# Kernel optimization log

Hardware: AMD Instinct MI355X
Metric: run time of the kernel (lower is better)

Reference implementation:

```python
import jax, jax.numpy as jnp
import numpy as np

B, L, D = 2, 2048, 1024
H = 16
HD = D // H  # 64


def setup_inputs() -> dict:
    key = jax.random.key(0)
    ks = jax.random.split(key, 7)
    s = 0.02
    return {
        "x": jax.random.normal(ks[0], (B, L, D), dtype=jnp.float32),
        "Wq": jax.random.normal(ks[1], (D, D), dtype=jnp.float32) * s,
        "bq": jnp.zeros((D,), dtype=jnp.float32),
        "Wkv": jax.random.normal(ks[2], (D, 2 * D), dtype=jnp.float32) * s,
        "bkv": jnp.zeros((2 * D,), dtype=jnp.float32),
        "Wo": jax.random.normal(ks[3], (D, D), dtype=jnp.float32) * s,
        "bo": jnp.zeros((D,), dtype=jnp.float32),
    }


def reference(x, Wq, bq, Wkv, bkv, Wo, bo):
    # q/kv projections (self-attention: key/value come from x)
    q = x @ Wq + bq                      # [B, L, D]
    kv = x @ Wkv + bkv                   # [B, L, 2D]
    k, v = jnp.split(kv, 2, axis=-1)     # each [B, L, D]
    # split heads: 'b l (h c) -> b h l c' (rope_embed_fraction=0 -> RoPE is identity)
    def heads(t):
        return t.reshape(B, L, H, HD).transpose(0, 2, 1, 3)
    qh, kh, vh = heads(q), heads(k), heads(v)   # [B, H, L, HD]
    scale = 1.0 / jnp.sqrt(jnp.asarray(HD, dtype=x.dtype))
    scores = jnp.einsum('bhqc,bhkc->bhqk', qh, kh) * scale  # [B, H, L, L]
    attn = jax.nn.softmax(scores, axis=-1)
    y = jnp.einsum('bhqk,bhkc->bhqc', attn, vh)             # [B, H, L, HD]
    # merge heads: 'b h l c -> b l (h c)'
    y = y.transpose(0, 2, 1, 3).reshape(B, L, D)
    return (y @ Wo + bo).reshape(x.shape)
```

## Files before the change

kernel.cpp:

```cpp
#include <hip/hip_runtime.h>

#define B_  2
#define L_  2048
#define D_  1024
#define H_  16
#define HD_ 64

typedef __attribute__((ext_vector_type(8))) short bf16x8;
typedef __attribute__((ext_vector_type(4))) float f32x4;
typedef __attribute__((ext_vector_type(16))) float f32x16;

#define MFMA16(a, b, c) __builtin_amdgcn_mfma_f32_16x16x32_bf16(a, b, c, 0, 0, 0)
#define MFMA32(a, b, c) __builtin_amdgcn_mfma_f32_32x32x16_bf16(a, b, c, 0, 0, 0)

__device__ __forceinline__ unsigned short f2bf(float f) {
    union { float f; unsigned u; } v; v.f = f;
    unsigned r = v.u + 0x7FFFu + ((v.u >> 16) & 1u);
    return (unsigned short)(r >> 16);
}

__device__ __forceinline__ unsigned pkbf(float a, float b) {
    union { float f; unsigned u; } x, y; x.f = a; y.f = b;
    return __builtin_amdgcn_perm(y.u, x.u, 0x07060302u);
}

__global__ __launch_bounds__(256) void convert_bf16(
    const float* __restrict__ in, unsigned short* __restrict__ out, int n4)
{
    for (int i = blockIdx.x * blockDim.x + threadIdx.x; i < n4;
         i += gridDim.x * blockDim.x) {
        float4 v = *(const float4*)(in + (size_t)i * 4);
        ushort4 u;
        u.x = f2bf(v.x); u.y = f2bf(v.y); u.z = f2bf(v.z); u.w = f2bf(v.w);
        *(ushort4*)(out + (size_t)i * 4) = u;
    }
}

__global__ __launch_bounds__(256) void prep_w(
    const float* __restrict__ Wq, const float* __restrict__ Wkv,
    const float* __restrict__ Wo,
    unsigned short* __restrict__ Wqt, unsigned short* __restrict__ Wkvt,
    unsigned short* __restrict__ Wot)
{
    __shared__ float t[32][33];
    const int z = blockIdx.z;
    const float* W;  unsigned short* Wt;  int N, nc;
    if (z == 0)      { W = Wq;  Wt = Wqt;  N = 1024; nc = 0; }
    else if (z == 1) { W = Wo;  Wt = Wot;  N = 1024; nc = 0; }
    else             { W = Wkv; Wt = Wkvt; N = 2048; nc = (z - 2) * 1024; }
    const int tx = threadIdx.x & 31, ty = threadIdx.x >> 5;
    const int n0 = nc + blockIdx.x * 32, k0 = blockIdx.y * 32;
    #pragma unroll
    for (int r = 0; r < 4; ++r)
        t[ty + r * 8][tx] = W[(size_t)(k0 + ty + r * 8) * N + n0 + tx];
    __syncthreads();
    #pragma unroll
    for (int r = 0; r < 4; ++r)
        Wt[(size_t)(n0 + ty + r * 8) * 1024 + k0 + tx] = f2bf(t[tx][ty + r * 8]);
}

__global__ __launch_bounds__(512, 1) void gemm_qkv8(
    const unsigned short* __restrict__ A,
    const unsigned short* __restrict__ Bt,
    const float* __restrict__ bq, const float* __restrict__ bkv,
    unsigned short* __restrict__ Qb, unsigned short* __restrict__ Kb,
    unsigned short* __restrict__ Vtg, float qscl)
{
    const int KDIM = 1024, NT = 16;
    __shared__ __align__(16) unsigned short lds[65536];

    const int tid = threadIdx.x;
    const int w = tid >> 6, l = tid & 63, g = l >> 4, ln = l & 15;
    const int wm = (w >> 2) & 1, wn = w & 3;

    const int lin = blockIdx.x;
    const int wg = (lin & 7) * 24 + (lin >> 3);
    const int by = wg / 12, bx = wg % 12;
    const int m0 = by * 256, n0 = bx * 256;

    const int sr8 = w * 8 + (l >> 3);
    const int sc  = (l & 7) ^ ((l >> 3) & 7);
    const unsigned short* Asrc = A  + (size_t)m0 * KDIM + sc * 8;
    const unsigned short* Bsrc = Bt + (size_t)n0 * KDIM + sc * 8;

#define SLOT_A(d, h) (lds + ((d) * 2 + (h)) * 8192)
#define SLOT_B(d, h) (lds + 32768 + ((d) * 2 + (h)) * 8192)

#define STG(slotp, srcp, hh, kt_) do {                                        \
    _Pragma("unroll")                                                         \
    for (int r_ = 0; r_ < 2; ++r_) {                                          \
        const int row_ = (hh) * 128 + r_ * 64 + sr8;                          \
        __builtin_amdgcn_global_load_lds(                                     \
            (const __attribute__((address_space(1))) void*)                   \
                ((srcp) + (size_t)row_ * KDIM + (kt_) * 64),                  \
            (__attribute__((address_space(3))) void*)                         \
                ((slotp) + r_ * 4096 + w * 512 + l * 8),                      \
            16, 0, 0);                                                        \
    }                                                                         \
} while (0)

    f32x4 acc[8][4];
    #pragma unroll
    for (int i = 0; i < 8; ++i)
        #pragma unroll
        for (int j = 0; j < 4; ++j) acc[i][j] = (f32x4){0.f, 0.f, 0.f, 0.f};

    bf16x8 aR[4][2], bB0[2][2], bB1[2][2];

    STG(SLOT_A(0, 0), Asrc, 0, 0);
    STG(SLOT_B(0, 1), Bsrc, 1, 0);
    STG(SLOT_A(0, 1), Asrc, 1, 0);
    STG(SLOT_B(0, 0), Bsrc, 0, 0);
    STG(SLOT_A(1, 0), Asrc, 0, 1);
    STG(SLOT_B(1, 1), Bsrc, 1, 1);

    #pragma unroll 1
    for (int kt = 0; kt < NT; ++kt) {
        const int cur = kt & 1, nxt = cur ^ 1;
        asm volatile("s_waitcnt vmcnt(4)" ::: "memory");
        __builtin_amdgcn_s_barrier();

        #pragma unroll
        for (int mi = 0; mi < 4; ++mi)
            #pragma unroll
            for (int kc = 0; kc < 2; ++kc) {
                const int rho = wm * 64 + mi * 16 + ln, c = kc * 4 + g;
                aR[mi][kc] = *(const bf16x8*)
                    (SLOT_A(cur, 0) + rho * 64 + ((c ^ (rho & 7)) * 8));
            }
        #pragma unroll
        for (int ni = 0; ni < 2; ++ni)
            #pragma unroll
            for (int kc = 0; kc < 2; ++kc) {
                const int rho = wn * 32 + ni * 16 + ln, c = kc * 4 + g;
                bB0[ni][kc] = *(const bf16x8*)
                    (SLOT_B(cur, 0) + rho * 64 + ((c ^ (rho & 7)) * 8));
            }
        if (kt + 1 < NT) STG(SLOT_A(nxt, 1), Asrc, 1, kt + 1);
        __builtin_amdgcn_s_barrier();
        asm volatile("s_waitcnt lgkmcnt(0)" ::: "memory");
        __builtin_amdgcn_s_setprio(1);
        #pragma unroll
        for (int mi = 0; mi < 4; ++mi)
            #pragma unroll
            for (int ni = 0; ni < 2; ++ni) {
                acc[mi][ni] = MFMA16(aR[mi][0], bB0[ni][0], acc[mi][ni]);
                acc[mi][ni] = MFMA16(aR[mi][1], bB0[ni][1], acc[mi][ni]);
            }
        __builtin_amdgcn_s_setprio(0);
        __builtin_amdgcn_s_barrier();

        #pragma unroll
        for (int ni = 0; ni < 2; ++ni)
            #pragma unroll
            for (int kc = 0; kc < 2; ++kc) {
                const int rho = wn * 32 + ni * 16 + ln, c = kc * 4 + g;
                bB1[ni][kc] = *(const bf16x8*)
                    (SLOT_B(cur, 1) + rho * 64 + ((c ^ (rho & 7)) * 8));
            }
        if (kt + 1 < NT) STG(SLOT_B(nxt, 0), Bsrc, 0, kt + 1);
        __builtin_amdgcn_s_barrier();
        asm volatile("s_waitcnt lgkmcnt(0)" ::: "memory");
        __builtin_amdgcn_s_setprio(1);
        #pragma unroll
        for (int mi = 0; mi < 4; ++mi)
            #pragma unroll
            for (int ni = 0; ni < 2; ++ni) {
                acc[mi][2 + ni] = MFMA16(aR[mi][0], bB1[ni][0], acc[mi][2 + ni]);
                acc[mi][2 + ni] = MFMA16(aR[mi][1], bB1[ni][1], acc[mi][2 + ni]);
            }
        __builtin_amdgcn_s_setprio(0);
        __builtin_amdgcn_s_barrier();

        #pragma unroll
        for (int mi = 0; mi < 4; ++mi)
            #pragma unroll
            for (int kc = 0; kc < 2; ++kc) {
                const int rho = wm * 64 + mi * 16 + ln, c = kc * 4 + g;
                aR[mi][kc] = *(const bf16x8*)
                    (SLOT_A(cur, 1) + rho * 64 + ((c ^ (rho & 7)) * 8));
            }
        if (kt + 2 < NT) STG(SLOT_A(cur, 0), Asrc, 0, kt + 2);
        __builtin_amdgcn_s_barrier();
        asm volatile("s_waitcnt lgkmcnt(0)" ::: "memory");
        __builtin_amdgcn_s_setprio(1);
        #pragma unroll
        for (int mi = 0; mi < 4; ++mi)
            #pragma unroll
            for (int ni = 0; ni < 2; ++ni) {
                acc[4 + mi][2 + ni] = MFMA16(aR[mi][0], bB1[ni][0], acc[4 + mi][2 + ni]);
                acc[4 + mi][2 + ni] = MFMA16(aR[mi][1], bB1[ni][1], acc[4 + mi][2 + ni]);
            }
        __builtin_amdgcn_s_setprio(0);
        __builtin_amdgcn_s_barrier();

        if (kt + 2 < NT) STG(SLOT_B(cur, 1), Bsrc, 1, kt + 2);
        __builtin_amdgcn_s_barrier();
        __builtin_amdgcn_s_setprio(1);
        #pragma unroll
        for (int mi = 0; mi < 4; ++mi)
            #pragma unroll
            for (int ni = 0; ni < 2; ++ni) {
                acc[4 + mi][ni] = MFMA16(aR[mi][0], bB0[ni][0], acc[4 + mi][ni]);
                acc[4 + mi][ni] = MFMA16(aR[mi][1], bB0[ni][1], acc[4 + mi][ni]);
            }
        __builtin_amdgcn_s_setprio(0);
        __builtin_amdgcn_s_barrier();
    }
#undef STG
#undef SLOT_A
#undef SLOT_B

    const int region = n0 >> 10;
    if (region == 2) {
        #pragma unroll
        for (int nh = 0; nh < 2; ++nh)
            #pragma unroll
            for (int ni = 0; ni < 2; ++ni) {
                const int d = n0 - 2048 + nh * 128 + wn * 32 + ni * 16 + ln;
                const float bv = bkv[1024 + d];
                #pragma unroll
                for (int mh = 0; mh < 2; ++mh)
                    #pragma unroll
                    for (int mi = 0; mi < 4; ++mi) {
                        const int tok = m0 + mh * 128 + wm * 64 + mi * 16 + g * 4;
                        const int bb = tok >> 11, t4 = tok & 2047;
                        const f32x4 av = acc[mh * 4 + mi][nh * 2 + ni];
                        ushort4 p4;
                        p4.x = f2bf(av[0] + bv); p4.y = f2bf(av[1] + bv);
                        p4.z = f2bf(av[2] + bv); p4.w = f2bf(av[3] + bv);
                        *(ushort4*)(Vtg + ((size_t)bb * 1024 + d) * 2048 + t4) = p4;
                    }
            }
    } else {
        const int isQ = (region == 0);
        const float osc = isQ ? qscl : 1.f;
        #pragma unroll
        for (int nh = 0; nh < 2; ++nh)
            #pragma unroll
            for (int ni = 0; ni < 2; ++ni) {
                const int col = n0 + nh * 128 + wn * 32 + ni * 16 + ln;
                const float bv = isQ ? bq[col] : bkv[col - 1024];
                const int ck = isQ ? col : col - 1024;
                #pragma unroll
                for (int mh = 0; mh < 2; ++mh)
                    #pragma unroll
                    for (int mi = 0; mi < 4; ++mi) {
                        const int row = m0 + mh * 128 + wm * 64 + mi * 16 + g * 4;
                        const f32x4 av = acc[mh * 4 + mi][nh * 2 + ni];
                        #pragma unroll
                        for (int r = 0; r < 4; ++r) {
                            const float vout = (av[r] + bv) * osc;
                            if (isQ)
                                Qb[(size_t)(row + r) * 1024 + ck] = f2bf(vout);
                            else
                                Kb[(size_t)(row + r) * 1024 + ck] = f2bf(vout);
                        }
                    }
            }
    }
}

__global__ __launch_bounds__(256) void gemm_bt(
    const unsigned short* __restrict__ A,
    const unsigned short* __restrict__ Bt,
    const float* __restrict__ bias,
    float* __restrict__ Cout, int M, int N, int K)
{
    __shared__ __align__(16) unsigned short As[128 * 32];
    __shared__ __align__(16) unsigned short Bs[128 * 32];
    const int tid = threadIdx.x;
    const int w = tid >> 6, l = tid & 63, g = l >> 4, ln = l & 15;
    const int wm = w >> 1, wn = w & 1;
    const int m0 = blockIdx.y * 128, n0 = blockIdx.x * 128;

    f32x4 acc[4][4];
    #pragma unroll
    for (int i = 0; i < 4; ++i)
        #pragma unroll
        for (int j = 0; j < 4; ++j) acc[i][j] = (f32x4){0.f, 0.f, 0.f, 0.f};

    const char* Ab = (const char*)A;
    const char* Bb = (const char*)Bt;
    const size_t strideK = (size_t)K * 2;

    for (int k0 = 0; k0 < K; k0 += 32) {
        #pragma unroll
        for (int i = 0; i < 2; ++i) {
            const int b = w * 2048 + i * 1024 + l * 16;
            const int row = b >> 6, cb = b & 63;
            __builtin_amdgcn_global_load_lds(
                (const __attribute__((address_space(1))) void*)
                    (Ab + (size_t)(m0 + row) * strideK + (size_t)k0 * 2 + cb),
                (__attribute__((address_space(3))) void*)
                    ((char*)As + w * 2048 + i * 1024),
                16, 0, 0);
            __builtin_amdgcn_global_load_lds(
                (const __attribute__((address_space(1))) void*)
                    (Bb + (size_t)(n0 + row) * strideK + (size_t)k0 * 2 + cb),
                (__attribute__((address_space(3))) void*)
                    ((char*)Bs + w * 2048 + i * 1024),
                16, 0, 0);
        }
        __syncthreads();
        bf16x8 af[4], bfr[4];
        #pragma unroll
        for (int m = 0; m < 4; ++m)
            af[m] = *(const bf16x8*)(As + (wm * 64 + m * 16 + ln) * 32 + g * 8);
        #pragma unroll
        for (int n = 0; n < 4; ++n)
            bfr[n] = *(const bf16x8*)(Bs + (wn * 64 + n * 16 + ln) * 32 + g * 8);
        #pragma unroll
        for (int m = 0; m < 4; ++m)
            #pragma unroll
            for (int n = 0; n < 4; ++n)
                acc[m][n] = MFMA16(af[m], bfr[n], acc[m][n]);
        __syncthreads();
    }

    #pragma unroll
    for (int n = 0; n < 4; ++n) {
        const int col = n0 + wn * 64 + n * 16 + ln;
        const float bv = bias[col];
        #pragma unroll
        for (int m = 0; m < 4; ++m) {
            const int row = m0 + wm * 64 + m * 16 + g * 4;
            #pragma unroll
            for (int r = 0; r < 4; ++r)
                Cout[(size_t)(row + r) * N + col] = acc[m][n][r] + bv;
        }
    }
}

__global__ __launch_bounds__(256) void attn_mfma(
    const unsigned short* __restrict__ Qb,
    const unsigned short* __restrict__ Kb,
    const unsigned short* __restrict__ Vtg,
    unsigned short* __restrict__ Yb)
{
    __shared__ __align__(16) unsigned short Ks[2][64 * 64];
    __shared__ __align__(16) unsigned short Vs[2][64 * 64];

    const int tid = threadIdx.x;
    const int w = tid >> 6, l = tid & 63;
    const int l31 = l & 31, hi = l >> 5, l7 = l & 7;
    const int dd = blockIdx.x;
    const int bid = (dd & 7) * 64 + (dd >> 3);
    const int qc = bid & 15, h = (bid >> 4) & 15, b = bid >> 8;
    const int qrow = b * L_ + qc * 128 + w * 32;

    const int sub = l >> 3;
    const int scc = (l & 7) ^ sub;
    const unsigned short* ksrc = Kb  + (size_t)(b * L_) * 1024 + h * HD_ + scc * 8;
    const unsigned short* vsrc = Vtg + (size_t)(b * D_ + h * HD_) * 2048 + scc * 8;

#define STAGE(jj, bb) do {                                                    \
    _Pragma("unroll")                                                         \
    for (int i_ = 0; i_ < 2; ++i_) {                                          \
        const int rowK = w * 16 + i_ * 8 + sub;                               \
        __builtin_amdgcn_global_load_lds(                                     \
            (const __attribute__((address_space(1))) void*)                   \
                (ksrc + (size_t)((jj) * 64 + rowK) * 1024),                   \
            (__attribute__((address_space(3))) void*)                         \
                (&Ks[bb][w * 1024 + i_ * 512]), 16, 0, 0);                    \
        __builtin_amdgcn_global_load_lds(                                     \
            (const __attribute__((address_space(1))) void*)                   \
                (vsrc + (size_t)rowK * 2048 + (jj) * 64),                     \
            (__attribute__((address_space(3))) void*)                         \
                (&Vs[bb][w * 1024 + i_ * 512]), 16, 0, 0);                    \
    }                                                                         \
} while (0)

    bf16x8 qa[4];
    #pragma unroll
    for (int dh = 0; dh < 4; ++dh)
        qa[dh] = *(const bf16x8*)
            (Qb + (size_t)(qrow + l31) * D_ + h * HD_ + dh * 16 + hi * 8);

    const f32x16 z16 = {0.f,0.f,0.f,0.f,0.f,0.f,0.f,0.f,
                        0.f,0.f,0.f,0.f,0.f,0.f,0.f,0.f};
    f32x16 o2[2], lacc;
    o2[0] = z16; o2[1] = z16; lacc = z16;

    const short one_s = (short)0x3F80;
    const bf16x8 ones = {one_s, one_s, one_s, one_s, one_s, one_s, one_s, one_s};

#define ATT_BODY(BUF, TNEXT, NBUF, DOSTG) do {                                \
    if (DOSTG) STAGE(TNEXT, NBUF);                                            \
    const unsigned short* Kc = &Ks[BUF][0];                                   \
    const unsigned short* Vc = &Vs[BUF][0];                                   \
          \
    bf16x8 kbf[2][4];                                                         \
    _Pragma("unroll")                                                         \
    for (int kk = 0; kk < 2; ++kk)                                            \
        _Pragma("unroll")                                                     \
        for (int dh = 0; dh < 4; ++dh)                                        \
            kbf[kk][dh] = *(const bf16x8*)                                    \
                (Kc + (kk * 32 + l31) * 64 + (((2 * dh + hi) ^ l7) * 8));     \
    f32x16 s2[2];                                                             \
    __builtin_amdgcn_s_setprio(1);                                            \
    _Pragma("unroll")                                                         \
    for (int kk = 0; kk < 2; ++kk) {                                          \
        s2[kk] = MFMA32(kbf[kk][0], qa[0], z16);                              \
        s2[kk] = MFMA32(kbf[kk][1], qa[1], s2[kk]);                           \
        s2[kk] = MFMA32(kbf[kk][2], qa[2], s2[kk]);                           \
        s2[kk] = MFMA32(kbf[kk][3], qa[3], s2[kk]);                           \
    }                                                                         \
    __builtin_amdgcn_s_setprio(0);                                            \
                                                    \
    _Pragma("unroll")                                                         \
    for (int kk = 0; kk < 2; ++kk)                                            \
        _Pragma("unroll")                                                     \
        for (int r = 0; r < 16; ++r)                                          \
            s2[kk][r] = __builtin_exp2f(s2[kk][r]);                           \
      \
    bf16x8 pa[4];                                                             \
    _Pragma("unroll")                                                         \
    for (int ks = 0; ks < 4; ++ks) {                                          \
        const int kk = ks >> 1, R = 8 * (ks & 1);                             \
        unsigned d0 = pkbf(s2[kk][R + 0], s2[kk][R + 1]);                     \
        unsigned d1 = pkbf(s2[kk][R + 2], s2[kk][R + 3]);                     \
        unsigned d2 = pkbf(s2[kk][R + 4], s2[kk][R + 5]);                     \
        unsigned d3 = pkbf(s2[kk][R + 6], s2[kk][R + 7]);                     \
               \
        asm volatile("v_permlane32_swap_b32 %0, %1" : "+v"(d0), "+v"(d2));    \
        asm volatile("v_permlane32_swap_b32 %0, %1" : "+v"(d1), "+v"(d3));    \
        union { unsigned u[4]; bf16x8 v; } pk_;                               \
        pk_.u[0] = d0; pk_.u[1] = d1; pk_.u[2] = d2; pk_.u[3] = d3;           \
        pa[ks] = pk_.v;                                                       \
    }                                                                         \
            \
    bf16x8 vbf[2][4];                                                         \
    _Pragma("unroll")                                                         \
    for (int dt = 0; dt < 2; ++dt)                                            \
        _Pragma("unroll")                                                     \
        for (int ks = 0; ks < 4; ++ks)                                        \
            vbf[dt][ks] = *(const bf16x8*)                                    \
                (Vc + (dt * 32 + l31) * 64 + (((2 * ks + hi) ^ l7) * 8));     \
    __builtin_amdgcn_s_setprio(1);                                            \
    _Pragma("unroll")                                                         \
    for (int dt = 0; dt < 2; ++dt)                                            \
        _Pragma("unroll")                                                     \
        for (int ks = 0; ks < 4; ++ks)                                        \
            o2[dt] = MFMA32(pa[ks], vbf[dt][ks], o2[dt]);                     \
    _Pragma("unroll")                                                         \
    for (int ks = 0; ks < 4; ++ks)                                            \
        lacc = MFMA32(pa[ks], ones, lacc);                                    \
    __builtin_amdgcn_s_setprio(0);                                            \
} while (0)

    STAGE(0, 0);
    __syncthreads();

    #pragma unroll 1
    for (int t = 0; t < L_ / 64; t += 2) {
        ATT_BODY(0, t + 1, 1, true);
        __syncthreads();
        ATT_BODY(1, t + 2, 0, (t + 2 < L_ / 64));
        __syncthreads();
    }
#undef ATT_BODY
#undef STAGE

    #pragma unroll
    for (int r = 0; r < 16; ++r) {
        const float inv = 1.f / lacc[r];
        const int row = qrow + (r & 3) + 8 * (r >> 2) + 4 * hi;
        #pragma unroll
        for (int dt = 0; dt < 2; ++dt)
            Yb[(size_t)row * D_ + h * HD_ + dt * 32 + l31] =
                f2bf(o2[dt][r] * inv);
    }
}

extern "C" void kernel_launch(void* const* d_in, const int* in_sizes, int n_in,
                              void* d_out, int out_size, void* d_ws, size_t ws_size,
                              hipStream_t stream)
{
    const float* x   = (const float*)d_in[0];
    const float* Wq  = (const float*)d_in[1];
    const float* bq  = (const float*)d_in[2];
    const float* Wkv = (const float*)d_in[3];
    const float* bkv = (const float*)d_in[4];
    const float* Wo  = (const float*)d_in[5];
    const float* bo  = (const float*)d_in[6];
    float* out = (float*)d_out;

    const int M = B_ * L_;
    unsigned short* ws = (unsigned short*)d_ws;
    unsigned short* xb   = ws;
    unsigned short* Wqt  = xb   + (size_t)M * D_;
    unsigned short* Wkvt = Wqt  + (size_t)D_ * D_;
    unsigned short* Wot  = Wkvt + (size_t)2 * D_ * D_;
    unsigned short* Qb   = Wot  + (size_t)D_ * D_;
    unsigned short* Kb   = Qb   + (size_t)M * D_;
    unsigned short* Vtg  = Kb   + (size_t)M * D_;
    unsigned short* Yb   = Vtg  + (size_t)B_ * D_ * L_;

    const float QSCL = 0.125f * 1.44269504089f;

    convert_bf16<<<2048, 256, 0, stream>>>(x, xb, M * D_ / 4);
    prep_w<<<dim3(32, 32, 4), 256, 0, stream>>>(Wq, Wkv, Wo, Wqt, Wkvt, Wot);

    gemm_qkv8<<<dim3(192), 512, 0, stream>>>(xb, Wqt, bq, bkv, Qb, Kb, Vtg, QSCL);

    attn_mfma<<<dim3(B_ * H_ * (L_ / 128)), 256, 0, stream>>>(Qb, Kb, Vtg, Yb);

    gemm_bt<<<dim3(D_ / 128, M / 128), 256, 0, stream>>>(Yb, Wot, bo, out, M, D_, D_);
}
```

Measured before the change: 137.9 us.

## Split attention over two KV halves with atomic accumulation and combine kernel

Splits the key/value sequence into two halves so the attention grid doubles from 512 to 1024 blocks. Each block accumulates an unnormalized output and row sum, and adds them into fp32 buffers with atomics. A new combine kernel then normalizes and converts the result to bf16. This aims to fill more CUs, at the cost of two memsets, fp32 atomic traffic and an extra kernel launch. It relies on there being no running max, so the partial sums can be added directly.

```diff
diff --git a/kernel.cpp b/kernel.cpp
--- a/kernel.cpp
+++ b/kernel.cpp
@@ -336,7 +336,7 @@
     const unsigned short* __restrict__ Qb,
     const unsigned short* __restrict__ Kb,
     const unsigned short* __restrict__ Vtg,
-    unsigned short* __restrict__ Yb)
+    float* __restrict__ Of, float* __restrict__ Lf)
 {
     __shared__ __align__(16) unsigned short Ks[2][64 * 64];
     __shared__ __align__(16) unsigned short Vs[2][64 * 64];
@@ -345,9 +345,11 @@
     const int w = tid >> 6, l = tid & 63;
     const int l31 = l & 31, hi = l >> 5, l7 = l & 7;
     const int dd = blockIdx.x;
-    const int bid = (dd & 7) * 64 + (dd >> 3);
-    const int qc = bid & 15, h = (bid >> 4) & 15, b = bid >> 8;
+    const int bid = (dd & 7) * 128 + (dd >> 3);
+    const int kh = bid & 1, qc = (bid >> 1) & 15;
+    const int h = (bid >> 5) & 15, b = bid >> 9;
     const int qrow = b * L_ + qc * 128 + w * 32;
+    const int kbase = kh * 16;
 
     const int sub = l >> 3;
     const int scc = (l & 7) ^ sub;
@@ -389,7 +391,6 @@
     if (DOSTG) STAGE(TNEXT, NBUF);                                            \
     const unsigned short* Kc = &Ks[BUF][0];                                   \
     const unsigned short* Vc = &Vs[BUF][0];                                   \
-          \
     bf16x8 kbf[2][4];                                                         \
     _Pragma("unroll")                                                         \
     for (int kk = 0; kk < 2; ++kk)                                            \
@@ -407,13 +408,11 @@
         s2[kk] = MFMA32(kbf[kk][3], qa[3], s2[kk]);                           \
     }                                                                         \
     __builtin_amdgcn_s_setprio(0);                                            \
-                                                    \
     _Pragma("unroll")                                                         \
     for (int kk = 0; kk < 2; ++kk)                                            \
         _Pragma("unroll")                                                     \
         for (int r = 0; r < 16; ++r)                                          \
             s2[kk][r] = __builtin_exp2f(s2[kk][r]);                           \
-      \
     bf16x8 pa[4];                                                             \
     _Pragma("unroll")                                                         \
     for (int ks = 0; ks < 4; ++ks) {                                          \
@@ -422,14 +421,12 @@
         unsigned d1 = pkbf(s2[kk][R + 2], s2[kk][R + 3]);                     \
         unsigned d2 = pkbf(s2[kk][R + 4], s2[kk][R + 5]);                     \
         unsigned d3 = pkbf(s2[kk][R + 6], s2[kk][R + 7]);                     \
-               \
         asm volatile("v_permlane32_swap_b32 %0, %1" : "+v"(d0), "+v"(d2));    \
         asm volatile("v_permlane32_swap_b32 %0, %1" : "+v"(d1), "+v"(d3));    \
         union { unsigned u[4]; bf16x8 v; } pk_;                               \
         pk_.u[0] = d0; pk_.u[1] = d1; pk_.u[2] = d2; pk_.u[3] = d3;           \
         pa[ks] = pk_.v;                                                       \
     }                                                                         \
-            \
     bf16x8 vbf[2][4];                                                         \
     _Pragma("unroll")                                                         \
     for (int dt = 0; dt < 2; ++dt)                                            \
@@ -449,14 +446,14 @@
     __builtin_amdgcn_s_setprio(0);                                            \
 } while (0)
 
-    STAGE(0, 0);
+    STAGE(kbase, 0);
     __syncthreads();
 
     #pragma unroll 1
-    for (int t = 0; t < L_ / 64; t += 2) {
-        ATT_BODY(0, t + 1, 1, true);
+    for (int t = 0; t < 16; t += 2) {
+        ATT_BODY(0, kbase + t + 1, 1, true);
         __syncthreads();
-        ATT_BODY(1, t + 2, 0, (t + 2 < L_ / 64));
+        ATT_BODY(1, kbase + t + 2, 0, (t + 2 < 16));
         __syncthreads();
     }
 #undef ATT_BODY
@@ -464,13 +461,28 @@
 
     #pragma unroll
     for (int r = 0; r < 16; ++r) {
-        const float inv = 1.f / lacc[r];
         const int row = qrow + (r & 3) + 8 * (r >> 2) + 4 * hi;
         #pragma unroll
         for (int dt = 0; dt < 2; ++dt)
-            Yb[(size_t)row * D_ + h * HD_ + dt * 32 + l31] =
-                f2bf(o2[dt][r] * inv);
-    }
+            atomicAdd(&Of[(size_t)row * D_ + h * HD_ + dt * 32 + l31], o2[dt][r]);
+        if (l31 == 0)
+            atomicAdd(&Lf[row * H_ + h], lacc[r]);
+    }
+}
+
+__global__ __launch_bounds__(256) void combine(
+    const float* __restrict__ Of, const float* __restrict__ Lf,
+    unsigned short* __restrict__ Yb)
+{
+    const int i = blockIdx.x * blockDim.x + threadIdx.x;
+    const int idx = i * 4;
+    const int row = idx >> 10, col = idx & 1023;
+    const float inv = 1.f / Lf[row * H_ + (col >> 6)];
+    float4 o = *(const float4*)(Of + idx);
+    ushort4 y;
+    y.x = f2bf(o.x * inv); y.y = f2bf(o.y * inv);
+    y.z = f2bf(o.z * inv); y.w = f2bf(o.w * inv);
+    *(ushort4*)(Yb + idx) = y;
 }
 
 extern "C" void kernel_launch(void* const* d_in, const int* in_sizes, int n_in,
@@ -495,7 +507,9 @@
     unsigned short* Qb   = Wot  + (size_t)D_ * D_;
     unsigned short* Kb   = Qb   + (size_t)M * D_;
     unsigned short* Vtg  = Kb   + (size_t)M * D_;
-    unsigned short* Yb   = Vtg  + (size_t)B_ * D_ * L_;
+    float* Of = (float*)(Vtg + (size_t)B_ * D_ * L_);
+    float* Lf = Of + (size_t)M * D_;
+    unsigned short* Yb = xb;
 
     const float QSCL = 0.125f * 1.44269504089f;
 
@@ -504,7 +518,13 @@
 
     gemm_qkv8<<<dim3(192), 512, 0, stream>>>(xb, Wqt, bq, bkv, Qb, Kb, Vtg, QSCL);
 
-    attn_mfma<<<dim3(B_ * H_ * (L_ / 128)), 256, 0, stream>>>(Qb, Kb, Vtg, Yb);
+    hipMemsetAsync(Of, 0, (size_t)M * D_ * 4, stream);
+    hipMemsetAsync(Lf, 0, (size_t)M * H_ * 4, stream);
+
+    attn_mfma<<<dim3(B_ * H_ * (L_ / 128) * 2), 256, 0, stream>>>(
+        Qb, Kb, Vtg, Of, Lf);
+
+    combine<<<dim3(M * D_ / 4 / 256), 256, 0, stream>>>(Of, Lf, Yb);
 
     gemm_bt<<<dim3(D_ / 128, M / 128), 256, 0, stream>>>(Yb, Wot, bo, out, M, D_, D_);
 }
```

Result: slower. 173.6 us (+25.9%).
